# Kernel optimization log

Measured on AMD Instinct MI355X. Metric: run time of the kernel, lower is better.

## Reference

```python
import jax, jax.numpy as jnp
import numpy as np

B = 32768
HID = 512          # hidden_dim
DIM = 256          # output dim
MAX_N = 17         # max_n + 1
KEY_MID = (MAX_N + HID) // 2   # 264
DEC_MID = (HID + DIM) // 2     # 384
SP_MID = (HID + MAX_N) // 2    # 264


def _linear_params(k, fan_in, fan_out):
    k1, k2 = jax.random.split(k)
    lim = 1.0 / np.sqrt(fan_in)
    W = jax.random.uniform(k1, (fan_in, fan_out), minval=-lim, maxval=lim, dtype=jnp.float32)
    b = jax.random.uniform(k2, (fan_out,), minval=-lim, maxval=lim, dtype=jnp.float32)
    return W, b


def setup_inputs() -> dict:
    key = jax.random.key(0)
    ks = jax.random.split(key, 7)
    z = jax.random.normal(ks[0], (B, HID), dtype=jnp.float32)
    key_W1, key_b1 = _linear_params(ks[1], MAX_N, KEY_MID)
    key_W2, key_b2 = _linear_params(ks[2], KEY_MID, HID)
    dec_W1, dec_b1 = _linear_params(ks[3], HID, DEC_MID)
    dec_W2, dec_b2 = _linear_params(ks[4], DEC_MID, DIM)
    sp_W1, sp_b1 = _linear_params(ks[5], HID, SP_MID)
    sp_W2, sp_b2 = _linear_params(ks[6], SP_MID, MAX_N)
    return dict(
        z=z,
        key_W1=key_W1, key_b1=key_b1,
        key_g1=jnp.ones((KEY_MID,), jnp.float32), key_be1=jnp.zeros((KEY_MID,), jnp.float32),
        key_W2=key_W2, key_b2=key_b2,
        dec_W1=dec_W1, dec_b1=dec_b1, dec_W2=dec_W2, dec_b2=dec_b2,
        sp_W1=sp_W1, sp_b1=sp_b1,
        sp_g1=jnp.ones((SP_MID,), jnp.float32), sp_be1=jnp.zeros((SP_MID,), jnp.float32),
        sp_W2=sp_W2, sp_b2=sp_b2,
    )


def _ln(x, g, b):
    m = x.mean(-1, keepdims=True)
    v = x.var(-1, keepdims=True)
    return (x - m) / jnp.sqrt(v + 1e-5) * g + b


def _ragged_indices(n):
    # n: np.int array [B]; returns batch ids and within-sample positions k
    n = np.asarray(n)
    batch = np.repeat(np.arange(n.shape[0]), n)
    starts = np.concatenate([np.zeros(1, dtype=np.int64), np.cumsum(n)[:-1]])
    k = np.arange(batch.shape[0]) - starts[batch]
    return batch, k


def reference(z, key_W1, key_b1, key_g1, key_be1, key_W2, key_b2,
              dec_W1, dec_b1, dec_W2, dec_b2,
              sp_W1, sp_b1, sp_g1, sp_be1, sp_W2, sp_b2):
    # size_pred MLP: Linear -> LayerNorm -> ReLU -> Linear
    h = jax.nn.relu(_ln(z @ sp_W1 + sp_b1, sp_g1, sp_be1))
    n_pred = h @ sp_W2 + sp_b2                       # [B, MAX_N]
    n = np.asarray(jnp.argmax(n_pred, axis=-1))      # concrete sizes (ragged)
    batch_np, k_np = _ragged_indices(n)
    batch = jnp.asarray(batch_np)
    k = jnp.asarray(k_np)
    pos = jax.nn.one_hot(k, MAX_N, dtype=jnp.float32)            # [T, MAX_N]
    # key_net: Linear -> LayerNorm -> ReLU -> Linear
    keys = jax.nn.relu(_ln(pos @ key_W1 + key_b1, key_g1, key_be1)) @ key_W2 + key_b2  # [T, HID]
    vals_rep = z[batch]                              # repeat_interleave via gather
    zp = vals_rep * keys
    # decoder: Linear -> ReLU -> Linear (no layernorm by default)
    x = jax.nn.relu(zp @ dec_W1 + dec_b1) @ dec_W2 + dec_b2      # [T, DIM]
    return x, batch
```

## Files before the change

kernel.cpp:

```cpp
#include <hip/hip_runtime.h>

#define B_N   32768
#define HID   512
#define DIM   256
#define MAXN  17
#define SM    264
#define DM    384

typedef __attribute__((ext_vector_type(8))) short bf16x8;
typedef __attribute__((ext_vector_type(4))) float f32x4;

static __device__ __forceinline__ unsigned short f2bf(float x) {
  union { float f; unsigned u; } v; v.f = x;
  unsigned r = (v.u + 0x7FFFu + ((v.u >> 16) & 1u)) >> 16;
  return (unsigned short)r;
}

__global__ __launch_bounds__(320) void sizepred_kernel(
    const float* __restrict__ z,  const float* __restrict__ W1,
    const float* __restrict__ b1, const float* __restrict__ g1,
    const float* __restrict__ be1, const float* __restrict__ W2,
    const float* __restrict__ b2, int* __restrict__ n_out)
{
  __shared__ __align__(16) float us[16 * 268];
  __shared__ __align__(16) float w2t[17 * 268];
  __shared__ float lnm[16], lnr[16];
  __shared__ float log17[16 * 17];

  const int tid = threadIdx.x;
  const int b0  = blockIdx.x * 16;

  for (int idx = tid; idx < 264 * 17; idx += 320) {
    int c = idx / 17, jj = idx - c * 17;
    w2t[jj * 268 + c] = W2[idx];
  }

  const bool act = tid < 264;
  const int  s0  = (tid / 66) * 4;
  const int  j0  = (tid % 66) * 4;

  float acc[4][4];
#pragma unroll
  for (int i = 0; i < 4; ++i)
#pragma unroll
    for (int q = 0; q < 4; ++q) acc[i][q] = 0.f;

  if (act) {
    const float* wp = W1 + j0;
    const float* zp = z + (size_t)(b0 + s0) * 512;
    for (int c0 = 0; c0 < 512; c0 += 8) {
      float a[4][8];
#pragma unroll
      for (int i = 0; i < 4; ++i) {
        float4 lo = *(const float4*)(zp + (size_t)i * 512 + c0);
        float4 hi = *(const float4*)(zp + (size_t)i * 512 + c0 + 4);
        a[i][0] = lo.x; a[i][1] = lo.y; a[i][2] = lo.z; a[i][3] = lo.w;
        a[i][4] = hi.x; a[i][5] = hi.y; a[i][6] = hi.z; a[i][7] = hi.w;
      }
#pragma unroll
      for (int cc = 0; cc < 8; ++cc) {
        float4 bv = *(const float4*)(wp + (size_t)(c0 + cc) * 264);
#pragma unroll
        for (int i = 0; i < 4; ++i) {
          acc[i][0] += a[i][cc] * bv.x;
          acc[i][1] += a[i][cc] * bv.y;
          acc[i][2] += a[i][cc] * bv.z;
          acc[i][3] += a[i][cc] * bv.w;
        }
      }
    }
    float4 bb = *(const float4*)&b1[j0];
#pragma unroll
    for (int i = 0; i < 4; ++i) {
      float4 o;
      o.x = acc[i][0] + bb.x; o.y = acc[i][1] + bb.y;
      o.z = acc[i][2] + bb.z; o.w = acc[i][3] + bb.w;
      *(float4*)&us[(s0 + i) * 268 + j0] = o;
    }
  }
  __syncthreads();

  if (tid < 16) {
    float s = 0.f, q = 0.f;
    for (int j = 0; j < 264; ++j) { float v = us[tid * 268 + j]; s += v; q += v * v; }
    float m   = s / 264.f;
    float var = q / 264.f - m * m;
    lnm[tid] = m;
    lnr[tid] = 1.f / sqrtf(var + 1e-5f);
  }
  __syncthreads();

  for (int idx = tid; idx < 16 * 264; idx += 320) {
    int s = idx / 264, j = idx - s * 264;
    float v = (us[s * 268 + j] - lnm[s]) * lnr[s] * g1[j] + be1[j];
    us[s * 268 + j] = fmaxf(v, 0.f);
  }
  __syncthreads();

  if (tid < 272) {
    int s = tid / 17, jj = tid - s * 17;
    float a = b2[jj];
    const float* up = &us[s * 268];
    const float* wt = &w2t[jj * 268];
#pragma unroll 4
    for (int c = 0; c < 264; c += 4) {
      float4 u = *(const float4*)(up + c);
      float4 w = *(const float4*)(wt + c);
      a += u.x * w.x; a += u.y * w.y; a += u.z * w.z; a += u.w * w.w;
    }
    log17[tid] = a;
  }
  __syncthreads();

  if (tid < 16) {
    int best = 0; float bv = log17[tid * 17];
    for (int jj = 1; jj < 17; ++jj) {
      float v = log17[tid * 17 + jj];
      if (v > bv) { bv = v; best = jj; }
    }
    n_out[b0 + tid] = best;
  }
}

__global__ __launch_bounds__(1024) void scan_kernel(const int* __restrict__ n,
                                                    int* __restrict__ starts)
{
  __shared__ int part[1024];
  const int tid  = threadIdx.x;
  const int base = tid * 32;
  int loc[32];
  int s = 0;
#pragma unroll
  for (int i = 0; i < 32; ++i) { loc[i] = n[base + i]; s += loc[i]; }
  part[tid] = s;
  __syncthreads();
  for (int off = 1; off < 1024; off <<= 1) {
    int v   = part[tid];
    int add = (tid >= off) ? part[tid - off] : 0;
    __syncthreads();
    part[tid] = v + add;
    __syncthreads();
  }
  int run = part[tid] - s;
#pragma unroll
  for (int i = 0; i < 32; ++i) { starts[base + i] = run; run += loc[i]; }
  if (tid == 1023) starts[B_N] = run;
}

__global__ __launch_bounds__(256) void scatter_kernel(
    const int* __restrict__ n, const int* __restrict__ starts,
    int* __restrict__ bi, int* __restrict__ ki, float* __restrict__ out, int T)
{
  int b = blockIdx.x * 256 + threadIdx.x;
  if (b >= B_N) return;
  int st = starts[b], nn = n[b];
  float* ob = out + (size_t)T * DIM;
  for (int k = 0; k < nn; ++k) {
    bi[st + k] = b;
    ki[st + k] = k;
    ob[st + k] = (float)b;
  }
}

__global__ __launch_bounds__(320) void keys_kernel(
    const float* __restrict__ W1, const float* __restrict__ b1,
    const float* __restrict__ g1, const float* __restrict__ be1,
    const float* __restrict__ W2, const float* __restrict__ b2,
    float* __restrict__ ktab)
{
  __shared__ float hs[264];
  __shared__ float mr[2];
  const int kk = blockIdx.x, tid = threadIdx.x;
  if (tid < 264) hs[tid] = W1[kk * 264 + tid] + b1[tid];
  __syncthreads();
  if (tid == 0) {
    float s = 0.f, q = 0.f;
    for (int j = 0; j < 264; ++j) { float v = hs[j]; s += v; q += v * v; }
    float m = s / 264.f;
    mr[0] = m;
    mr[1] = 1.f / sqrtf(q / 264.f - m * m + 1e-5f);
  }
  __syncthreads();
  if (tid < 264) hs[tid] = fmaxf((hs[tid] - mr[0]) * mr[1] * g1[tid] + be1[tid], 0.f);
  __syncthreads();
  for (int c = tid; c < 512; c += 320) {
    float a = b2[c];
    for (int j = 0; j < 264; ++j) a += hs[j] * W2[j * 512 + c];
    ktab[kk * 512 + c] = a;
  }
}

__global__ __launch_bounds__(64) void pack_kernel(
    const float* __restrict__ W1, const float* __restrict__ W2,
    short* __restrict__ W1p, short* __restrict__ W2p)
{
  const int g = blockIdx.x, l = threadIdx.x;
  const float* W; int nt, kt, N;
  if (g < 384) { W = W1; kt = g / 24; nt = g % 24; N = 384; }
  else         { W = W2; int gg = g - 384; kt = gg / 16; nt = gg % 16; N = 256; }
  const int krow = kt * 32 + ((l >> 4) << 3);
  const int col  = nt * 16 + (l & 15);
  short v[8];
#pragma unroll
  for (int j = 0; j < 8; ++j)
    v[j] = (short)f2bf(W[(size_t)(krow + j) * N + col]);
  short* d = (g < 384) ? (W1p + ((size_t)g * 64 + l) * 8)
                       : (W2p + ((size_t)(g - 384) * 64 + l) * 8);
  *(bf16x8*)d = *(bf16x8*)v;
}

__global__ __launch_bounds__(256) void decoder_kernel(
    const float* __restrict__ z,  const float* __restrict__ ktab,
    const short* __restrict__ W1p, const float* __restrict__ b1,
    const short* __restrict__ W2p, const float* __restrict__ b2,
    const int* __restrict__ bi,   const int* __restrict__ ki,
    float* __restrict__ out, int T)
{
  __shared__ __align__(16) short zps[32768];
  __shared__ int tb[64], tk[64];

  const int tid  = threadIdx.x;
  const int wave = tid >> 6;
  const int lane = tid & 63;
  const int t0   = blockIdx.x * 64;

  if (tid < 64) {
    int t = t0 + tid;
    tb[tid] = (t < T) ? bi[t] : 0;
    tk[tid] = (t < T) ? ki[t] : 0;
  }
  __syncthreads();

#pragma unroll 4
  for (int it = 0; it < 16; ++it) {
    int chunk = tid + it * 256;
    int l  = chunk & 63;
    int mt = (chunk >> 6) & 3;
    int kt = chunk >> 8;
    int m  = mt * 16 + (l & 15);
    int k0 = kt * 32 + ((l >> 4) << 3);
    const float4* zr = (const float4*)(z    + (size_t)tb[m] * 512 + k0);
    const float4* kr = (const float4*)(ktab + (size_t)tk[m] * 512 + k0);
    float4 z0 = zr[0], z1 = zr[1], k4 = kr[0], k5 = kr[1];
    short v[8];
    v[0] = (short)f2bf(z0.x * k4.x); v[1] = (short)f2bf(z0.y * k4.y);
    v[2] = (short)f2bf(z0.z * k4.z); v[3] = (short)f2bf(z0.w * k4.w);
    v[4] = (short)f2bf(z1.x * k5.x); v[5] = (short)f2bf(z1.y * k5.y);
    v[6] = (short)f2bf(z1.z * k5.z); v[7] = (short)f2bf(z1.w * k5.w);
    *(bf16x8*)&zps[(size_t)chunk * 8] = *(bf16x8*)v;
  }
  __syncthreads();

  f32x4 acc[4][6];
#pragma unroll
  for (int mt = 0; mt < 4; ++mt)
#pragma unroll
    for (int j = 0; j < 6; ++j) acc[mt][j] = (f32x4){0.f, 0.f, 0.f, 0.f};

  {
    const short* wb = W1p + ((size_t)(wave * 6) * 64 + lane) * 8;
#pragma unroll 2
    for (int kt = 0; kt < 16; ++kt) {
      bf16x8 a0 = *(bf16x8*)&zps[((kt * 4 + 0) * 64 + lane) * 8];
      bf16x8 a1 = *(bf16x8*)&zps[((kt * 4 + 1) * 64 + lane) * 8];
      bf16x8 a2 = *(bf16x8*)&zps[((kt * 4 + 2) * 64 + lane) * 8];
      bf16x8 a3 = *(bf16x8*)&zps[((kt * 4 + 3) * 64 + lane) * 8];
#pragma unroll
      for (int j = 0; j < 6; ++j) {
        bf16x8 bf = *(const bf16x8*)(wb + (size_t)kt * 12288 + j * 512);
        acc[0][j] = __builtin_amdgcn_mfma_f32_16x16x32_bf16(a0, bf, acc[0][j], 0, 0, 0);
        acc[1][j] = __builtin_amdgcn_mfma_f32_16x16x32_bf16(a1, bf, acc[1][j], 0, 0, 0);
        acc[2][j] = __builtin_amdgcn_mfma_f32_16x16x32_bf16(a2, bf, acc[2][j], 0, 0, 0);
        acc[3][j] = __builtin_amdgcn_mfma_f32_16x16x32_bf16(a3, bf, acc[3][j], 0, 0, 0);
      }
    }
  }
  __syncthreads();

  {
    short* Hs = zps;
    float bload[6];
#pragma unroll
    for (int j = 0; j < 6; ++j)
      bload[j] = b1[wave * 96 + j * 16 + (lane & 15)];
#pragma unroll
    for (int mt = 0; mt < 4; ++mt) {
#pragma unroll
      for (int j = 0; j < 6; ++j) {
        int c = wave * 96 + j * 16 + (lane & 15);
        int lane2hi = ((c >> 3) & 3) << 4;
        int ktp = (c >> 5) * 4;
        int jj = c & 7;
#pragma unroll
        for (int r = 0; r < 4; ++r) {
          int m = mt * 16 + (lane >> 4) * 4 + r;
          float v = fmaxf(acc[mt][j][r] + bload[j], 0.f);
          Hs[((ktp + (m >> 4)) * 64 + ((m & 15) | lane2hi)) * 8 + jj] = (short)f2bf(v);
        }
      }
    }
  }
  __syncthreads();

  f32x4 acc2[4][4];
#pragma unroll
  for (int mt = 0; mt < 4; ++mt)
#pragma unroll
    for (int j = 0; j < 4; ++j) acc2[mt][j] = (f32x4){0.f, 0.f, 0.f, 0.f};

  {
    const short* Hs = zps;
    const short* wb = W2p + ((size_t)(wave * 4) * 64 + lane) * 8;
#pragma unroll 2
    for (int kt = 0; kt < 12; ++kt) {
      bf16x8 a0 = *(const bf16x8*)&Hs[((kt * 4 + 0) * 64 + lane) * 8];
      bf16x8 a1 = *(const bf16x8*)&Hs[((kt * 4 + 1) * 64 + lane) * 8];
      bf16x8 a2 = *(const bf16x8*)&Hs[((kt * 4 + 2) * 64 + lane) * 8];
      bf16x8 a3 = *(const bf16x8*)&Hs[((kt * 4 + 3) * 64 + lane) * 8];
#pragma unroll
      for (int j = 0; j < 4; ++j) {
        bf16x8 bf = *(const bf16x8*)(wb + (size_t)kt * 8192 + j * 512);
        acc2[0][j] = __builtin_amdgcn_mfma_f32_16x16x32_bf16(a0, bf, acc2[0][j], 0, 0, 0);
        acc2[1][j] = __builtin_amdgcn_mfma_f32_16x16x32_bf16(a1, bf, acc2[1][j], 0, 0, 0);
        acc2[2][j] = __builtin_amdgcn_mfma_f32_16x16x32_bf16(a2, bf, acc2[2][j], 0, 0, 0);
        acc2[3][j] = __builtin_amdgcn_mfma_f32_16x16x32_bf16(a3, bf, acc2[3][j], 0, 0, 0);
      }
    }
  }

  {
    float bload[4];
#pragma unroll
    for (int j = 0; j < 4; ++j)
      bload[j] = b2[wave * 64 + j * 16 + (lane & 15)];
#pragma unroll
    for (int mt = 0; mt < 4; ++mt) {
#pragma unroll
      for (int r = 0; r < 4; ++r) {
        int t = t0 + mt * 16 + (lane >> 4) * 4 + r;
        if (t < T) {
#pragma unroll
          for (int j = 0; j < 4; ++j) {
            int c = wave * 64 + j * 16 + (lane & 15);
            out[(size_t)t * 256 + c] = acc2[mt][j][r] + bload[j];
          }
        }
      }
    }
  }
}

extern "C" void kernel_launch(void* const* d_in, const int* in_sizes, int n_in,
                              void* d_out, int out_size, void* d_ws, size_t ws_size,
                              hipStream_t stream)
{
  const float* z      = (const float*)d_in[0];
  const float* keyW1  = (const float*)d_in[1];
  const float* keyb1  = (const float*)d_in[2];
  const float* keyg1  = (const float*)d_in[3];
  const float* keybe1 = (const float*)d_in[4];
  const float* keyW2  = (const float*)d_in[5];
  const float* keyb2  = (const float*)d_in[6];
  const float* decW1  = (const float*)d_in[7];
  const float* decb1  = (const float*)d_in[8];
  const float* decW2  = (const float*)d_in[9];
  const float* decb2  = (const float*)d_in[10];
  const float* spW1   = (const float*)d_in[11];
  const float* spb1   = (const float*)d_in[12];
  const float* spg1   = (const float*)d_in[13];
  const float* spbe1  = (const float*)d_in[14];
  const float* spW2   = (const float*)d_in[15];
  const float* spb2   = (const float*)d_in[16];

  const int T = out_size / (DIM + 1);

  char* ws = (char*)d_ws;
  int*   n_arr  = (int*)(ws);
  int*   starts = (int*)(ws + 131072);
  float* ktab   = (float*)(ws + 262160);
  short* W1p    = (short*)(ws + 296976);
  short* W2p    = (short*)(ws + 690192);
  int*   bi     = (int*)(ws + 886800);
  size_t kioff  = 886800 + (((size_t)T * 4 + 15) / 16) * 16;
  int*   ki     = (int*)(ws + kioff);

  float* outF = (float*)d_out;

  sizepred_kernel<<<B_N / 16, 320, 0, stream>>>(z, spW1, spb1, spg1, spbe1, spW2, spb2, n_arr);
  pack_kernel<<<576, 64, 0, stream>>>(decW1, decW2, W1p, W2p);
  scan_kernel<<<1, 1024, 0, stream>>>(n_arr, starts);
  keys_kernel<<<MAXN, 320, 0, stream>>>(keyW1, keyb1, keyg1, keybe1, keyW2, keyb2, ktab);
  scatter_kernel<<<B_N / 256, 256, 0, stream>>>(n_arr, starts, bi, ki, outF, T);
  if (T > 0)
    decoder_kernel<<<(T + 63) / 64, 256, 0, stream>>>(z, ktab, W1p, decb1, W2p, decb2, bi, ki, outF, T);
}
```

Measured before the change: 1.265 ms.

## Halve decoder row tile, drop sizepred W2 staging, vectorize scan I/O

The decoder now handles 32 rows per block instead of 64, which halves its shared memory (32KB) and accumulators and adds a launch bound of 4 blocks per CU for higher occupancy. It also uses packed bf16 conversion intrinsics. The cost is that each block rereads the full weight set from L2 for half as many rows, roughly doubling weight traffic. The sizepred kernel no longer stages W2 transposed in shared memory and instead reads strided from global, and the scan kernel loads and stores with int4 vectors.

```diff
diff --git a/kernel.cpp b/kernel.cpp
--- a/kernel.cpp
+++ b/kernel.cpp
@@ -1,4 +1,5 @@
 #include <hip/hip_runtime.h>
+#include <hip/hip_bf16.h>
 
 #define B_N   32768
 #define HID   512
@@ -16,6 +17,12 @@
   return (unsigned short)r;
 }
 
+static __device__ __forceinline__ unsigned pkbf(float a, float b) {
+  __hip_bfloat162 h = __float22bfloat162_rn(float2{a, b});
+  union { __hip_bfloat162 h; unsigned u; } cv; cv.h = h;
+  return cv.u;
+}
+
 __global__ __launch_bounds__(320) void sizepred_kernel(
     const float* __restrict__ z,  const float* __restrict__ W1,
     const float* __restrict__ b1, const float* __restrict__ g1,
@@ -23,17 +30,11 @@
     const float* __restrict__ b2, int* __restrict__ n_out)
 {
   __shared__ __align__(16) float us[16 * 268];
-  __shared__ __align__(16) float w2t[17 * 268];
   __shared__ float lnm[16], lnr[16];
   __shared__ float log17[16 * 17];
 
   const int tid = threadIdx.x;
   const int b0  = blockIdx.x * 16;
-
-  for (int idx = tid; idx < 264 * 17; idx += 320) {
-    int c = idx / 17, jj = idx - c * 17;
-    w2t[jj * 268 + c] = W2[idx];
-  }
 
   const bool act = tid < 264;
   const int  s0  = (tid / 66) * 4;
@@ -101,12 +102,13 @@
     int s = tid / 17, jj = tid - s * 17;
     float a = b2[jj];
     const float* up = &us[s * 268];
-    const float* wt = &w2t[jj * 268];
 #pragma unroll 4
     for (int c = 0; c < 264; c += 4) {
       float4 u = *(const float4*)(up + c);
-      float4 w = *(const float4*)(wt + c);
-      a += u.x * w.x; a += u.y * w.y; a += u.z * w.z; a += u.w * w.w;
+      a += u.x * W2[(c + 0) * 17 + jj];
+      a += u.y * W2[(c + 1) * 17 + jj];
+      a += u.z * W2[(c + 2) * 17 + jj];
+      a += u.w * W2[(c + 3) * 17 + jj];
     }
     log17[tid] = a;
   }
@@ -131,7 +133,12 @@
   int loc[32];
   int s = 0;
 #pragma unroll
-  for (int i = 0; i < 32; ++i) { loc[i] = n[base + i]; s += loc[i]; }
+  for (int i = 0; i < 8; ++i) {
+    int4 v = ((const int4*)(n + base))[i];
+    loc[i * 4 + 0] = v.x; loc[i * 4 + 1] = v.y;
+    loc[i * 4 + 2] = v.z; loc[i * 4 + 3] = v.w;
+    s += v.x + v.y + v.z + v.w;
+  }
   part[tid] = s;
   __syncthreads();
   for (int off = 1; off < 1024; off <<= 1) {
@@ -143,7 +150,14 @@
   }
   int run = part[tid] - s;
 #pragma unroll
-  for (int i = 0; i < 32; ++i) { starts[base + i] = run; run += loc[i]; }
+  for (int i = 0; i < 8; ++i) {
+    int4 w;
+    w.x = run; run += loc[i * 4 + 0];
+    w.y = run; run += loc[i * 4 + 1];
+    w.z = run; run += loc[i * 4 + 2];
+    w.w = run; run += loc[i * 4 + 3];
+    ((int4*)(starts + base))[i] = w;
+  }
   if (tid == 1023) starts[B_N] = run;
 }
 
@@ -209,69 +223,65 @@
   *(bf16x8*)d = *(bf16x8*)v;
 }
 
-__global__ __launch_bounds__(256) void decoder_kernel(
+__global__ __launch_bounds__(256, 4) void decoder_kernel(
     const float* __restrict__ z,  const float* __restrict__ ktab,
     const short* __restrict__ W1p, const float* __restrict__ b1,
     const short* __restrict__ W2p, const float* __restrict__ b2,
     const int* __restrict__ bi,   const int* __restrict__ ki,
     float* __restrict__ out, int T)
 {
-  __shared__ __align__(16) short zps[32768];
-  __shared__ int tb[64], tk[64];
+  __shared__ __align__(16) short zps[16384];
+  __shared__ int tb[32], tk[32];
 
   const int tid  = threadIdx.x;
   const int wave = tid >> 6;
   const int lane = tid & 63;
-  const int t0   = blockIdx.x * 64;
-
-  if (tid < 64) {
+  const int t0   = blockIdx.x * 32;
+
+  if (tid < 32) {
     int t = t0 + tid;
     tb[tid] = (t < T) ? bi[t] : 0;
     tk[tid] = (t < T) ? ki[t] : 0;
   }
   __syncthreads();
 
-#pragma unroll 4
-  for (int it = 0; it < 16; ++it) {
+#pragma unroll
+  for (int it = 0; it < 8; ++it) {
     int chunk = tid + it * 256;
     int l  = chunk & 63;
-    int mt = (chunk >> 6) & 3;
-    int kt = chunk >> 8;
+    int mt = (chunk >> 6) & 1;
+    int kt = chunk >> 7;
     int m  = mt * 16 + (l & 15);
     int k0 = kt * 32 + ((l >> 4) << 3);
     const float4* zr = (const float4*)(z    + (size_t)tb[m] * 512 + k0);
     const float4* kr = (const float4*)(ktab + (size_t)tk[m] * 512 + k0);
     float4 z0 = zr[0], z1 = zr[1], k4 = kr[0], k5 = kr[1];
-    short v[8];
-    v[0] = (short)f2bf(z0.x * k4.x); v[1] = (short)f2bf(z0.y * k4.y);
-    v[2] = (short)f2bf(z0.z * k4.z); v[3] = (short)f2bf(z0.w * k4.w);
-    v[4] = (short)f2bf(z1.x * k5.x); v[5] = (short)f2bf(z1.y * k5.y);
-    v[6] = (short)f2bf(z1.z * k5.z); v[7] = (short)f2bf(z1.w * k5.w);
-    *(bf16x8*)&zps[(size_t)chunk * 8] = *(bf16x8*)v;
-  }
-  __syncthreads();
-
-  f32x4 acc[4][6];
-#pragma unroll
-  for (int mt = 0; mt < 4; ++mt)
+    uint4 u;
+    u.x = pkbf(z0.x * k4.x, z0.y * k4.y);
+    u.y = pkbf(z0.z * k4.z, z0.w * k4.w);
+    u.z = pkbf(z1.x * k5.x, z1.y * k5.y);
+    u.w = pkbf(z1.z * k5.z, z1.w * k5.w);
+    *(uint4*)&zps[(size_t)chunk * 8] = u;
+  }
+  __syncthreads();
+
+  f32x4 acc[2][6];
+#pragma unroll
+  for (int mt = 0; mt < 2; ++mt)
 #pragma unroll
     for (int j = 0; j < 6; ++j) acc[mt][j] = (f32x4){0.f, 0.f, 0.f, 0.f};
 
   {
     const short* wb = W1p + ((size_t)(wave * 6) * 64 + lane) * 8;
-#pragma unroll 2
+#pragma unroll 4
     for (int kt = 0; kt < 16; ++kt) {
-      bf16x8 a0 = *(bf16x8*)&zps[((kt * 4 + 0) * 64 + lane) * 8];
-      bf16x8 a1 = *(bf16x8*)&zps[((kt * 4 + 1) * 64 + lane) * 8];
-      bf16x8 a2 = *(bf16x8*)&zps[((kt * 4 + 2) * 64 + lane) * 8];
-      bf16x8 a3 = *(bf16x8*)&zps[((kt * 4 + 3) * 64 + lane) * 8];
+      bf16x8 a0 = *(bf16x8*)&zps[((kt * 2 + 0) * 64 + lane) * 8];
+      bf16x8 a1 = *(bf16x8*)&zps[((kt * 2 + 1) * 64 + lane) * 8];
 #pragma unroll
       for (int j = 0; j < 6; ++j) {
         bf16x8 bf = *(const bf16x8*)(wb + (size_t)kt * 12288 + j * 512);
         acc[0][j] = __builtin_amdgcn_mfma_f32_16x16x32_bf16(a0, bf, acc[0][j], 0, 0, 0);
         acc[1][j] = __builtin_amdgcn_mfma_f32_16x16x32_bf16(a1, bf, acc[1][j], 0, 0, 0);
-        acc[2][j] = __builtin_amdgcn_mfma_f32_16x16x32_bf16(a2, bf, acc[2][j], 0, 0, 0);
-        acc[3][j] = __builtin_amdgcn_mfma_f32_16x16x32_bf16(a3, bf, acc[3][j], 0, 0, 0);
       }
     }
   }
@@ -284,46 +294,48 @@
     for (int j = 0; j < 6; ++j)
       bload[j] = b1[wave * 96 + j * 16 + (lane & 15)];
 #pragma unroll
-    for (int mt = 0; mt < 4; ++mt) {
+    for (int mt = 0; mt < 2; ++mt) {
 #pragma unroll
       for (int j = 0; j < 6; ++j) {
         int c = wave * 96 + j * 16 + (lane & 15);
         int lane2hi = ((c >> 3) & 3) << 4;
-        int ktp = (c >> 5) * 4;
+        int koff = (c >> 5) * 2;
         int jj = c & 7;
-#pragma unroll
-        for (int r = 0; r < 4; ++r) {
-          int m = mt * 16 + (lane >> 4) * 4 + r;
-          float v = fmaxf(acc[mt][j][r] + bload[j], 0.f);
-          Hs[((ktp + (m >> 4)) * 64 + ((m & 15) | lane2hi)) * 8 + jj] = (short)f2bf(v);
-        }
-      }
-    }
-  }
-  __syncthreads();
-
-  f32x4 acc2[4][4];
-#pragma unroll
-  for (int mt = 0; mt < 4; ++mt)
+        int mbase = mt * 16 + (lane >> 4) * 4;
+        int a0 = ((koff + (mbase >> 4)) * 64 + ((mbase & 15) | lane2hi)) * 8 + jj;
+        float v0 = fmaxf(acc[mt][j][0] + bload[j], 0.f);
+        float v1 = fmaxf(acc[mt][j][1] + bload[j], 0.f);
+        float v2 = fmaxf(acc[mt][j][2] + bload[j], 0.f);
+        float v3 = fmaxf(acc[mt][j][3] + bload[j], 0.f);
+        unsigned p01 = pkbf(v0, v1);
+        unsigned p23 = pkbf(v2, v3);
+        Hs[a0 +  0] = (short)(p01 & 0xFFFFu);
+        Hs[a0 +  8] = (short)(p01 >> 16);
+        Hs[a0 + 16] = (short)(p23 & 0xFFFFu);
+        Hs[a0 + 24] = (short)(p23 >> 16);
+      }
+    }
+  }
+  __syncthreads();
+
+  f32x4 acc2[2][4];
+#pragma unroll
+  for (int mt = 0; mt < 2; ++mt)
 #pragma unroll
     for (int j = 0; j < 4; ++j) acc2[mt][j] = (f32x4){0.f, 0.f, 0.f, 0.f};
 
   {
     const short* Hs = zps;
     const short* wb = W2p + ((size_t)(wave * 4) * 64 + lane) * 8;
-#pragma unroll 2
+#pragma unroll 4
     for (int kt = 0; kt < 12; ++kt) {
-      bf16x8 a0 = *(const bf16x8*)&Hs[((kt * 4 + 0) * 64 + lane) * 8];
-      bf16x8 a1 = *(const bf16x8*)&Hs[((kt * 4 + 1) * 64 + lane) * 8];
-      bf16x8 a2 = *(const bf16x8*)&Hs[((kt * 4 + 2) * 64 + lane) * 8];
-      bf16x8 a3 = *(const bf16x8*)&Hs[((kt * 4 + 3) * 64 + lane) * 8];
+      bf16x8 a0 = *(const bf16x8*)&Hs[((kt * 2 + 0) * 64 + lane) * 8];
+      bf16x8 a1 = *(const bf16x8*)&Hs[((kt * 2 + 1) * 64 + lane) * 8];
 #pragma unroll
       for (int j = 0; j < 4; ++j) {
         bf16x8 bf = *(const bf16x8*)(wb + (size_t)kt * 8192 + j * 512);
         acc2[0][j] = __builtin_amdgcn_mfma_f32_16x16x32_bf16(a0, bf, acc2[0][j], 0, 0, 0);
         acc2[1][j] = __builtin_amdgcn_mfma_f32_16x16x32_bf16(a1, bf, acc2[1][j], 0, 0, 0);
-        acc2[2][j] = __builtin_amdgcn_mfma_f32_16x16x32_bf16(a2, bf, acc2[2][j], 0, 0, 0);
-        acc2[3][j] = __builtin_amdgcn_mfma_f32_16x16x32_bf16(a3, bf, acc2[3][j], 0, 0, 0);
       }
     }
   }
@@ -334,7 +346,7 @@
     for (int j = 0; j < 4; ++j)
       bload[j] = b2[wave * 64 + j * 16 + (lane & 15)];
 #pragma unroll
-    for (int mt = 0; mt < 4; ++mt) {
+    for (int mt = 0; mt < 2; ++mt) {
 #pragma unroll
       for (int r = 0; r < 4; ++r) {
         int t = t0 + mt * 16 + (lane >> 4) * 4 + r;
@@ -392,5 +404,5 @@
   keys_kernel<<<MAXN, 320, 0, stream>>>(keyW1, keyb1, keyg1, keybe1, keyW2, keyb2, ktab);
   scatter_kernel<<<B_N / 256, 256, 0, stream>>>(n_arr, starts, bi, ki, outF, T);
   if (T > 0)
-    decoder_kernel<<<(T + 63) / 64, 256, 0, stream>>>(z, ktab, W1p, decb1, W2p, decb2, bi, ki, outF, T);
-}
+    decoder_kernel<<<(T + 31) / 32, 256, 0, stream>>>(z, ktab, W1p, decb1, W2p, decb2, bi, ki, outF, T);
+}
```

After: 1.280 ms. No clear change (+1.2%).
